# Kernel optimization log

Measured on AMD Instinct MI355X. Metric: run time of the kernel, lower is better.

## Reference

```python
import math
import jax, jax.numpy as jnp
import numpy as np

NUM_HEADS = 16
QUERY_SIZE = 1024
SEQ = 2048
HEAD = QUERY_SIZE // NUM_HEADS  # qk_size = vo_size = 64


def setup_inputs() -> dict:
    key = jax.random.key(0)
    ks = jax.random.split(key, 8)
    s = 0.02
    query = jax.random.normal(ks[0], (SEQ, QUERY_SIZE), jnp.float32)
    key_ = jax.random.normal(ks[1], (SEQ, QUERY_SIZE), jnp.float32)
    value = jax.random.normal(ks[2], (SEQ, QUERY_SIZE), jnp.float32)
    # causal mask (mask='causal' with state=None -> offset 0)
    mask = jnp.tril(jnp.ones((SEQ, SEQ), dtype=bool))
    Wq = jax.random.normal(ks[3], (QUERY_SIZE, QUERY_SIZE), jnp.float32) * s
    Wk = jax.random.normal(ks[4], (QUERY_SIZE, QUERY_SIZE), jnp.float32) * s
    Wv = jax.random.normal(ks[5], (QUERY_SIZE, QUERY_SIZE), jnp.float32) * s
    Wo = jax.random.normal(ks[6], (QUERY_SIZE, QUERY_SIZE), jnp.float32) * s
    return {"query": query, "key_": key_, "value": value, "mask": mask,
            "Wq": Wq, "Wk": Wk, "Wv": Wv, "Wo": Wo}


def reference(query, key_, value, mask, Wq, Wk, Wv, Wo):
    H, D = NUMS = NUM_HEADS, HEAD
    S = query.shape[0]
    inv_sqrt_d = 1.0 / math.sqrt(D)
    # per-token linear projections, split into heads: [S, H, D]
    q = (query @ Wq.T).reshape(S, H, D)
    k = (key_ @ Wk.T).reshape(S, H, D)
    v = (value @ Wv.T).reshape(S, H, D)
    # NOTE: original divides BOTH q and k by sqrt(d) (effective 1/d scaling)
    q = q * inv_sqrt_d
    k = k * inv_sqrt_d
    # logits per head: [H, S, S]
    logits = jnp.einsum('shd,Shd->hsS', q, k)
    logits = jnp.where(mask[None, :, :], logits, jnp.finfo(logits.dtype).min)
    # per-head GLOBAL max subtraction, softmax in fp32, cast back (faithful)
    m = jnp.max(logits, axis=(1, 2), keepdims=True)
    weights = jax.nn.softmax((logits - m).astype(jnp.float32), axis=-1).astype(query.dtype)
    attn = jnp.einsum('hsS,ShD->shD', weights, v).reshape(S, H * D)
    return attn @ Wo.T
```

## Files before the change

### kernel.cpp

```cpp
#include <hip/hip_runtime.h>
#include <hip/hip_bf16.h>

typedef __bf16 bf16_t;
typedef __bf16 bf16x8 __attribute__((ext_vector_type(8)));
typedef float f32x4 __attribute__((ext_vector_type(4)));

#define MFMA(A, B, C) __builtin_amdgcn_mfma_f32_16x16x32_bf16(A, B, C, 0, 0, 0)

#define GLL16(g, l) __builtin_amdgcn_global_load_lds(                      \
    (const __attribute__((address_space(1))) void*)(g),                    \
    (__attribute__((address_space(3))) void*)(l), 16, 0, 0)

__global__ __launch_bounds__(256) void cvt_all(
    const float* __restrict__ q, const float* __restrict__ k, const float* __restrict__ v,
    const float* __restrict__ wq, const float* __restrict__ wk,
    const float* __restrict__ wv, const float* __restrict__ wo,
    bf16_t* __restrict__ xq, bf16_t* __restrict__ xk, bf16_t* __restrict__ xv,
    bf16_t* __restrict__ ywq, bf16_t* __restrict__ ywk,
    bf16_t* __restrict__ ywv, bf16_t* __restrict__ ywo)
{
  const long gid = (long)blockIdx.x * 256 + threadIdx.x;
  const float* s; bf16_t* d; long off; float sc = 1.0f;
  if (gid < 262144)       { s = q;  d = xq;  off = gid; }
  else if (gid < 524288)  { s = k;  d = xk;  off = gid - 262144; }
  else if (gid < 786432)  { s = v;  d = xv;  off = gid - 524288; }
  else if (gid < 917504)  { s = wq; d = ywq; off = gid - 786432;  sc = 0.125f; }
  else if (gid < 1048576) { s = wk; d = ywk; off = gid - 917504;  sc = 0.125f * 1.44269504f; }
  else if (gid < 1179648) { s = wv; d = ywv; off = gid - 1048576; }
  else                    { s = wo; d = ywo; off = gid - 1179648; }
  const float* p = s + off * 8;
  float4 a = *(const float4*)p, b = *(const float4*)(p + 4);
  bf16x8 o;
  o[0] = (bf16_t)(a.x * sc); o[1] = (bf16_t)(a.y * sc);
  o[2] = (bf16_t)(a.z * sc); o[3] = (bf16_t)(a.w * sc);
  o[4] = (bf16_t)(b.x * sc); o[5] = (bf16_t)(b.y * sc);
  o[6] = (bf16_t)(b.z * sc); o[7] = (bf16_t)(b.w * sc);
  *(bf16x8*)(d + off * 8) = o;
}

__device__ __forceinline__ void gemm_core(const bf16_t* __restrict__ A,
                                          const bf16_t* __restrict__ W,
                                          int bm, int bn,
                                          bf16_t (&As)[2][128 * 64],
                                          bf16_t (&Bs)[2][64 * 64],
                                          f32x4 (&acc)[4][2])
{
  const int tid = threadIdx.x, lane = tid & 63, wave = tid >> 6;
  const int l15 = lane & 15, l4 = lane >> 4, l7 = l15 & 7;
  const int wm = (wave >> 1) * 64, wn = (wave & 1) * 32;

  auto stage = [&](int buf, int k0) {
#pragma unroll
    for (int i = 0; i < 4; ++i) {
      const int id = i * 256 + tid, row = id >> 3, cph = id & 7;
      GLL16(A + (size_t)(bm + row) * 1024 + k0 + 8 * (cph ^ (row & 7)),
            &As[buf][(i * 256 + wave * 64) * 8]);
    }
#pragma unroll
    for (int i = 0; i < 2; ++i) {
      const int id = i * 256 + tid, row = id >> 3, cph = id & 7;
      GLL16(W + (size_t)(bn + row) * 1024 + k0 + 8 * (cph ^ (row & 7)),
            &Bs[buf][(i * 256 + wave * 64) * 8]);
    }
  };

  stage(0, 0);
#pragma unroll
  for (int s = 0; s < 16; ++s) {
    if (s + 1 < 16) stage((s + 1) & 1, (s + 1) * 64);
    __syncthreads();
    const bf16_t* as = As[s & 1];
    const bf16_t* bs = Bs[s & 1];
#pragma unroll
    for (int ks = 0; ks < 2; ++ks) {
      bf16x8 af[4], bfr[2];
#pragma unroll
      for (int i = 0; i < 4; ++i)
        af[i] = *(const bf16x8*)(&as[(wm + i * 16 + l15) * 64 + 8 * ((ks * 4 + l4) ^ l7)]);
#pragma unroll
      for (int j = 0; j < 2; ++j)
        bfr[j] = *(const bf16x8*)(&bs[(wn + j * 16 + l15) * 64 + 8 * ((ks * 4 + l4) ^ l7)]);
#pragma unroll
      for (int i = 0; i < 4; ++i)
#pragma unroll
        for (int j = 0; j < 2; ++j)
          acc[i][j] = MFMA(af[i], bfr[j], acc[i][j]);
    }
    __syncthreads();
  }
}

__global__ __launch_bounds__(256) void gemm_qkv(
    const bf16_t* __restrict__ xq, const bf16_t* __restrict__ xk, const bf16_t* __restrict__ xv,
    const bf16_t* __restrict__ ywq, const bf16_t* __restrict__ ywk, const bf16_t* __restrict__ ywv,
    bf16_t* __restrict__ qo, bf16_t* __restrict__ ko, bf16_t* __restrict__ vt)
{
  __shared__ __align__(16) bf16_t As[2][128 * 64];
  __shared__ __align__(16) bf16_t Bs[2][64 * 64];
  const int z = blockIdx.z;
  const bf16_t* A = z == 0 ? xq : z == 1 ? xk : xv;
  const bf16_t* W = z == 0 ? ywq : z == 1 ? ywk : ywv;
  const int bm = blockIdx.x * 128, bn = blockIdx.y * 64;
  f32x4 acc[4][2] = {};
  gemm_core(A, W, bm, bn, As, Bs, acc);
  const int tid = threadIdx.x, lane = tid & 63, wave = tid >> 6;
  const int l15 = lane & 15, l4 = lane >> 4;
  const int wm = (wave >> 1) * 64, wn = (wave & 1) * 32;
  if (z < 2) {
    bf16_t* C = z == 0 ? qo : ko;
#pragma unroll
    for (int i = 0; i < 4; ++i)
#pragma unroll
      for (int j = 0; j < 2; ++j)
#pragma unroll
        for (int r = 0; r < 4; ++r)
          C[(size_t)(bm + wm + i * 16 + 4 * l4 + r) * 1024 + bn + wn + j * 16 + l15] =
              (bf16_t)acc[i][j][r];
  } else {
#pragma unroll
    for (int i = 0; i < 4; ++i)
#pragma unroll
      for (int j = 0; j < 2; ++j)
#pragma unroll
        for (int r = 0; r < 4; ++r)
          vt[(size_t)(bn + wn + j * 16 + l15) * 2048 + bm + wm + i * 16 + 4 * l4 + r] =
              (bf16_t)acc[i][j][r];
  }
}

__global__ __launch_bounds__(256) void gemm_out(
    const bf16_t* __restrict__ ctx, const bf16_t* __restrict__ ywo, float* __restrict__ out)
{
  __shared__ __align__(16) bf16_t As[2][128 * 64];
  __shared__ __align__(16) bf16_t Bs[2][64 * 64];
  const int bm = blockIdx.x * 128, bn = blockIdx.y * 64;
  f32x4 acc[4][2] = {};
  gemm_core(ctx, ywo, bm, bn, As, Bs, acc);
  const int tid = threadIdx.x, lane = tid & 63, wave = tid >> 6;
  const int l15 = lane & 15, l4 = lane >> 4;
  const int wm = (wave >> 1) * 64, wn = (wave & 1) * 32;
#pragma unroll
  for (int i = 0; i < 4; ++i)
#pragma unroll
    for (int j = 0; j < 2; ++j)
#pragma unroll
      for (int r = 0; r < 4; ++r)
        out[(size_t)(bm + wm + i * 16 + 4 * l4 + r) * 1024 + bn + wn + j * 16 + l15] =
            acc[i][j][r];
}

__global__ __launch_bounds__(512) void attn512v2(
    const bf16_t* __restrict__ Qb, const bf16_t* __restrict__ Kb,
    const bf16_t* __restrict__ Vt, bf16_t* __restrict__ Ctx)
{
  __shared__ __align__(16) char pool[16384 + 16384 + 10240 + 256];
  bf16_t* KsP = (bf16_t*)pool;
  bf16_t* VsP = (bf16_t*)(pool + 16384);
  bf16_t* PsP = (bf16_t*)(pool + 32768);
  float*  Osc = (float*)pool;
  float*  Dsc = (float*)(pool + 43008);

  const int bid = blockIdx.x;
  const int qt = 31 - (bid >> 4);
  const int h = bid & 15;
  const int hoff = h * 64;
  const int tid = threadIdx.x, lane = tid & 63, wave = tid >> 6;
  const int qg = wave & 3, kh = wave >> 2;
  const int l15 = lane & 15, l4 = lane >> 4, l7 = l15 & 7;

  const int qb = qt * 64;
  const int nch = qt + 1;
  const int qmin = qb + 16 * qg;

  bf16x8 qf[2];
#pragma unroll
  for (int kc = 0; kc < 2; ++kc)
    qf[kc] = *(const bf16x8*)(Qb + (size_t)(qb + 16 * qg + l15) * 1024 + hoff + 32 * kc + 8 * l4);

  f32x4 oacc[4] = {};
  float den[4] = {0.f, 0.f, 0.f, 0.f};

  bf16x8 rk, rv;
  auto issue = [&](int c) {
    const int t0 = c * 64;
    const int kr = tid >> 3, kc = tid & 7;
    rk = *(const bf16x8*)(Kb + (size_t)(t0 + kr) * 1024 + hoff + 8 * kc);
    rv = *(const bf16x8*)(Vt + (size_t)(hoff + kr) * 2048 + t0 + 8 * kc);
  };
  auto commit = [&](int buf) {
    const int kr = tid >> 3, kc = tid & 7;
    *(bf16x8*)(&KsP[buf * 4096 + kr * 64 + 8 * (kc ^ (kr & 7))]) = rk;
    *(bf16x8*)(&VsP[buf * 4096 + kr * 64 + 8 * (kc ^ (kr & 7))]) = rv;
  };

  bf16_t* Pw = &PsP[wave * 640];
  auto PROC = [&](int cur, int c, auto masked) {
    const int tb = c * 64 + kh * 32;
    if (tb > qmin + 15) return;
    const bf16_t* Ksb = KsP + cur * 4096;
    const bf16_t* Vsb = VsP + cur * 4096;
    f32x4 sv[2] = {};
#pragma unroll
    for (int tf = 0; tf < 2; ++tf) {
      const int krow = 32 * kh + 16 * tf + l15;
      bf16x8 kf0 = *(const bf16x8*)(&Ksb[krow * 64 + 8 * (l4 ^ l7)]);
      bf16x8 kf1 = *(const bf16x8*)(&Ksb[krow * 64 + 8 * ((4 + l4) ^ l7)]);
      sv[tf] = MFMA(qf[0], kf0, sv[tf]);
      sv[tf] = MFMA(qf[1], kf1, sv[tf]);
    }
#pragma unroll
    for (int tf = 0; tf < 2; ++tf) {
      const int t = tb + 16 * tf + l15;
#pragma unroll
      for (int r = 0; r < 4; ++r) {
        float p = __builtin_amdgcn_exp2f(sv[tf][r]);
        if constexpr (decltype(masked)::value) {
          const int qq = qb + 16 * qg + 4 * l4 + r;
          p = (t <= qq) ? p : 0.0f;
        }
        den[r] += p;
        Pw[(4 * l4 + r) * 40 + 16 * tf + l15] = (bf16_t)p;
      }
    }
    asm volatile("s_waitcnt lgkmcnt(0)" ::: "memory");
    bf16x8 pa = *(const bf16x8*)(&Pw[l15 * 40 + 8 * l4]);
#pragma unroll
    for (int df = 0; df < 4; ++df) {
      const int vrow = 16 * df + l15;
      bf16x8 vf = *(const bf16x8*)(&Vsb[vrow * 64 + 8 * ((4 * kh + l4) ^ l7)]);
      oacc[df] = MFMA(pa, vf, oacc[df]);
    }
  };

  issue(0);
  commit(0);
  int cur = 0;
  for (int c = 0; c < nch; ++c) {
    const bool pre = (c + 1 < nch);
    if (pre) issue(c + 1);
    __syncthreads();
    const int tb = c * 64 + kh * 32;
    if (tb + 31 <= qmin)
      PROC(cur, c, std::integral_constant<bool, false>{});
    else
      PROC(cur, c, std::integral_constant<bool, true>{});
    if (pre) commit(cur ^ 1);
    cur ^= 1;
  }

#pragma unroll
  for (int r = 0; r < 4; ++r)
#pragma unroll
    for (int m = 1; m < 16; m <<= 1)
      den[r] += __shfl_xor(den[r], m, 64);

  __syncthreads();
  if (kh == 1) {
    const int rl = qg * 16 + 4 * l4;
#pragma unroll
    for (int r = 0; r < 4; ++r) {
#pragma unroll
      for (int df = 0; df < 4; ++df)
        Osc[(rl + r) * 66 + 16 * df + l15] = oacc[df][r];
      if (l15 == 0) Dsc[rl + r] = den[r];
    }
  }
  __syncthreads();
  if (kh == 0) {
#pragma unroll
    for (int r = 0; r < 4; ++r) {
      const int row = qg * 16 + 4 * l4 + r;
      const float inv = 1.0f / (den[r] + Dsc[row]);
#pragma unroll
      for (int df = 0; df < 4; ++df) {
        const int col = 16 * df + l15;
        const float s = oacc[df][r] + Osc[row * 66 + col];
        Ctx[(size_t)(qb + row) * 1024 + hoff + col] = (bf16_t)(s * inv);
      }
    }
  }
}

extern "C" void kernel_launch(void* const* d_in, const int* in_sizes, int n_in,
                              void* d_out, int out_size, void* d_ws, size_t ws_size,
                              hipStream_t stream)
{
  const float* query = (const float*)d_in[0];
  const float* key_  = (const float*)d_in[1];
  const float* value = (const float*)d_in[2];
  const float* Wq = (const float*)d_in[4];
  const float* Wk = (const float*)d_in[5];
  const float* Wv = (const float*)d_in[6];
  const float* Wo = (const float*)d_in[7];
  float* out = (float*)d_out;

  const size_t SE = (size_t)2048 * 1024, EE = (size_t)1024 * 1024;
  bf16_t* xq  = (bf16_t*)d_ws;
  bf16_t* xk  = xq + SE;
  bf16_t* xv  = xk + SE;
  bf16_t* wq  = xv + SE;
  bf16_t* wk  = wq + EE;
  bf16_t* wv  = wk + EE;
  bf16_t* wo  = wv + EE;
  bf16_t* qo  = wo + EE;
  bf16_t* ko  = qo + SE;
  bf16_t* vt  = ko + SE;
  bf16_t* ctx = vt + SE;

  cvt_all<<<5120, 256, 0, stream>>>(query, key_, value, Wq, Wk, Wv, Wo,
                                    xq, xk, xv, wq, wk, wv, wo);
  gemm_qkv<<<dim3(16, 16, 3), 256, 0, stream>>>(xq, xk, xv, wq, wk, wv, qo, ko, vt);
  attn512v2<<<512, 512, 0, stream>>>(qo, ko, vt, ctx);
  gemm_out<<<dim3(16, 16), 256, 0, stream>>>(ctx, wo, out);
}
```

Before: 75.58 us.

## Rewrite attention as register-resident 32x32 MFMA kernel with split-K waves

Replaces the LDS-staged attention kernel with one where each wave loads K and V fragments straight from global memory into registers, double-buffered. It uses 32x32x16 MFMAs and moves the P tile between lane halves with shuffles instead of through LDS. Query tiles shrink to 32 rows, giving 1024 blocks of 4 waves, and each wave takes every fourth key chunk; partial outputs and denominators are reduced through shared memory at the end. This removes per-chunk __syncthreads and LDS traffic, at the cost of redundant global/L2 loads across waves and more registers.

```diff
diff --git a/kernel.cpp b/kernel.cpp
--- a/kernel.cpp
+++ b/kernel.cpp
@@ -4,12 +4,25 @@
 typedef __bf16 bf16_t;
 typedef __bf16 bf16x8 __attribute__((ext_vector_type(8)));
 typedef float f32x4 __attribute__((ext_vector_type(4)));
+typedef float f32x16 __attribute__((ext_vector_type(16)));
 
 #define MFMA(A, B, C) __builtin_amdgcn_mfma_f32_16x16x32_bf16(A, B, C, 0, 0, 0)
+#define MFMA32(A, B, C) __builtin_amdgcn_mfma_f32_32x32x16_bf16(A, B, C, 0, 0, 0)
 
 #define GLL16(g, l) __builtin_amdgcn_global_load_lds(                      \
     (const __attribute__((address_space(1))) void*)(g),                    \
     (__attribute__((address_space(3))) void*)(l), 16, 0, 0)
+
+static __device__ __forceinline__ bf16x8 frag4(unsigned a, unsigned b, unsigned c, unsigned d) {
+  union { unsigned u[4]; bf16x8 v; } x;
+  x.u[0] = a; x.u[1] = b; x.u[2] = c; x.u[3] = d;
+  return x.v;
+}
+static __device__ __forceinline__ unsigned pack2b(bf16_t lo, bf16_t hi) {
+  union { bf16_t b[2]; unsigned u; } x;
+  x.b[0] = lo; x.b[1] = hi;
+  return x.u;
+}
 
 __global__ __launch_bounds__(256) void cvt_all(
     const float* __restrict__ q, const float* __restrict__ k, const float* __restrict__ v,
@@ -149,134 +162,119 @@
             acc[i][j][r];
 }
 
-__global__ __launch_bounds__(512) void attn512v2(
+__global__ __launch_bounds__(256) void attn_reg(
     const bf16_t* __restrict__ Qb, const bf16_t* __restrict__ Kb,
     const bf16_t* __restrict__ Vt, bf16_t* __restrict__ Ctx)
 {
-  __shared__ __align__(16) char pool[16384 + 16384 + 10240 + 256];
-  bf16_t* KsP = (bf16_t*)pool;
-  bf16_t* VsP = (bf16_t*)(pool + 16384);
-  bf16_t* PsP = (bf16_t*)(pool + 32768);
-  float*  Osc = (float*)pool;
-  float*  Dsc = (float*)(pool + 43008);
+  __shared__ float Osc[3][32 * 64];
+  __shared__ float Dsc[4][32];
 
   const int bid = blockIdx.x;
-  const int qt = 31 - (bid >> 4);
+  const int u = 63 - (bid >> 4);
   const int h = bid & 15;
   const int hoff = h * 64;
-  const int tid = threadIdx.x, lane = tid & 63, wave = tid >> 6;
-  const int qg = wave & 3, kh = wave >> 2;
-  const int l15 = lane & 15, l4 = lane >> 4, l7 = l15 & 7;
-
-  const int qb = qt * 64;
-  const int nch = qt + 1;
-  const int qmin = qb + 16 * qg;
-
-  bf16x8 qf[2];
-#pragma unroll
-  for (int kc = 0; kc < 2; ++kc)
-    qf[kc] = *(const bf16x8*)(Qb + (size_t)(qb + 16 * qg + l15) * 1024 + hoff + 32 * kc + 8 * l4);
-
-  f32x4 oacc[4] = {};
-  float den[4] = {0.f, 0.f, 0.f, 0.f};
-
-  bf16x8 rk, rv;
-  auto issue = [&](int c) {
-    const int t0 = c * 64;
-    const int kr = tid >> 3, kc = tid & 7;
-    rk = *(const bf16x8*)(Kb + (size_t)(t0 + kr) * 1024 + hoff + 8 * kc);
-    rv = *(const bf16x8*)(Vt + (size_t)(hoff + kr) * 2048 + t0 + 8 * kc);
+  const int lane = threadIdx.x & 63, tph = threadIdx.x >> 6;
+  const int l31 = lane & 31, hi = lane >> 5;
+
+  const int qb = u * 32;
+  const int q_lane = qb + l31;
+  const int nch = u + 1;
+  const bf16_t* Kh = Kb + hoff;
+  const bf16_t* Vh = Vt + (size_t)hoff * 2048;
+
+  bf16x8 qf[4];
+#pragma unroll
+  for (int st = 0; st < 4; ++st)
+    qf[st] = *(const bf16x8*)(Qb + (size_t)(qb + l31) * 1024 + hoff + 16 * st + 8 * hi);
+
+  f32x16 o0 = {}, o1 = {};
+  float den = 0.f;
+
+  bf16x8 kfA[4], vfA[4], kfB[4], vfB[4];
+  auto LOAD = [&](bf16x8 (&kf)[4], bf16x8 (&vf)[4], int c) {
+    const int t0 = c * 32;
+#pragma unroll
+    for (int st = 0; st < 4; ++st)
+      kf[st] = *(const bf16x8*)(Kh + (size_t)(t0 + l31) * 1024 + 16 * st + 8 * hi);
+#pragma unroll
+    for (int db = 0; db < 2; ++db)
+#pragma unroll
+      for (int kh = 0; kh < 2; ++kh)
+        vf[db * 2 + kh] = *(const bf16x8*)(Vh + (size_t)(32 * db + l31) * 2048 + t0 + 16 * kh + 8 * hi);
   };
-  auto commit = [&](int buf) {
-    const int kr = tid >> 3, kc = tid & 7;
-    *(bf16x8*)(&KsP[buf * 4096 + kr * 64 + 8 * (kc ^ (kr & 7))]) = rk;
-    *(bf16x8*)(&VsP[buf * 4096 + kr * 64 + 8 * (kc ^ (kr & 7))]) = rv;
+
+  auto PROC = [&](const bf16x8 (&kf)[4], const bf16x8 (&vf)[4], int c) {
+    const int t0 = c * 32;
+    f32x16 sv = {};
+#pragma unroll
+    for (int st = 0; st < 4; ++st)
+      sv = MFMA32(kf[st], qf[st], sv);
+    const bool diag = (c + 1 == nch);
+    bf16_t pb[16];
+#pragma unroll
+    for (int reg = 0; reg < 16; ++reg) {
+      const int t = t0 + (reg & 3) + 8 * (reg >> 2) + 4 * hi;
+      float e = __builtin_amdgcn_exp2f(sv[reg]);
+      if (diag && t > q_lane) e = 0.f;
+      const bf16_t b = (bf16_t)e;
+      pb[reg] = b;
+      den += (float)b;
+    }
+    unsigned pk[8];
+#pragma unroll
+    for (int i = 0; i < 8; ++i) pk[i] = pack2b(pb[2 * i], pb[2 * i + 1]);
+    const unsigned r0a = __shfl_xor((int)(hi ? pk[0] : pk[2]), 32, 64);
+    const unsigned r0b = __shfl_xor((int)(hi ? pk[1] : pk[3]), 32, 64);
+    const unsigned r1a = __shfl_xor((int)(hi ? pk[4] : pk[6]), 32, 64);
+    const unsigned r1b = __shfl_xor((int)(hi ? pk[5] : pk[7]), 32, 64);
+    const bf16x8 pf0 = hi ? frag4(r0a, r0b, pk[2], pk[3]) : frag4(pk[0], pk[1], r0a, r0b);
+    const bf16x8 pf1 = hi ? frag4(r1a, r1b, pk[6], pk[7]) : frag4(pk[4], pk[5], r1a, r1b);
+    o0 = MFMA32(pf0, vf[0], o0);
+    o0 = MFMA32(pf1, vf[1], o0);
+    o1 = MFMA32(pf0, vf[2], o1);
+    o1 = MFMA32(pf1, vf[3], o1);
   };
 
-  bf16_t* Pw = &PsP[wave * 640];
-  auto PROC = [&](int cur, int c, auto masked) {
-    const int tb = c * 64 + kh * 32;
-    if (tb > qmin + 15) return;
-    const bf16_t* Ksb = KsP + cur * 4096;
-    const bf16_t* Vsb = VsP + cur * 4096;
-    f32x4 sv[2] = {};
-#pragma unroll
-    for (int tf = 0; tf < 2; ++tf) {
-      const int krow = 32 * kh + 16 * tf + l15;
-      bf16x8 kf0 = *(const bf16x8*)(&Ksb[krow * 64 + 8 * (l4 ^ l7)]);
-      bf16x8 kf1 = *(const bf16x8*)(&Ksb[krow * 64 + 8 * ((4 + l4) ^ l7)]);
-      sv[tf] = MFMA(qf[0], kf0, sv[tf]);
-      sv[tf] = MFMA(qf[1], kf1, sv[tf]);
-    }
-#pragma unroll
-    for (int tf = 0; tf < 2; ++tf) {
-      const int t = tb + 16 * tf + l15;
-#pragma unroll
-      for (int r = 0; r < 4; ++r) {
-        float p = __builtin_amdgcn_exp2f(sv[tf][r]);
-        if constexpr (decltype(masked)::value) {
-          const int qq = qb + 16 * qg + 4 * l4 + r;
-          p = (t <= qq) ? p : 0.0f;
-        }
-        den[r] += p;
-        Pw[(4 * l4 + r) * 40 + 16 * tf + l15] = (bf16_t)p;
-      }
-    }
+  int c = tph;
+  if (c < nch) {
+    LOAD(kfA, vfA, c);
+    while (true) {
+      if (c + 4 < nch) LOAD(kfB, vfB, c + 4);
+      PROC(kfA, vfA, c);
+      c += 4;
+      if (c >= nch) break;
+      if (c + 4 < nch) LOAD(kfA, vfA, c + 4);
+      PROC(kfB, vfB, c);
+      c += 4;
+      if (c >= nch) break;
+    }
+  }
+
+  den += __shfl_xor(den, 32, 64);
+
+  if (hi == 0) Dsc[tph][l31] = den;
+  if (tph > 0) {
+#pragma unroll
+    for (int reg = 0; reg < 16; ++reg) {
+      const int qr = (reg & 3) + 8 * (reg >> 2) + 4 * hi;
+      Osc[tph - 1][qr * 64 + l31] = o0[reg];
+      Osc[tph - 1][qr * 64 + 32 + l31] = o1[reg];
+    }
+  }
+  __syncthreads();
+  if (tph == 0) {
+    const float dtot = Dsc[0][l31] + Dsc[1][l31] + Dsc[2][l31] + Dsc[3][l31];
+    if (hi == 0) Dsc[0][l31] = dtot;
     asm volatile("s_waitcnt lgkmcnt(0)" ::: "memory");
-    bf16x8 pa = *(const bf16x8*)(&Pw[l15 * 40 + 8 * l4]);
-#pragma unroll
-    for (int df = 0; df < 4; ++df) {
-      const int vrow = 16 * df + l15;
-      bf16x8 vf = *(const bf16x8*)(&Vsb[vrow * 64 + 8 * ((4 * kh + l4) ^ l7)]);
-      oacc[df] = MFMA(pa, vf, oacc[df]);
-    }
-  };
-
-  issue(0);
-  commit(0);
-  int cur = 0;
-  for (int c = 0; c < nch; ++c) {
-    const bool pre = (c + 1 < nch);
-    if (pre) issue(c + 1);
-    __syncthreads();
-    const int tb = c * 64 + kh * 32;
-    if (tb + 31 <= qmin)
-      PROC(cur, c, std::integral_constant<bool, false>{});
-    else
-      PROC(cur, c, std::integral_constant<bool, true>{});
-    if (pre) commit(cur ^ 1);
-    cur ^= 1;
-  }
-
-#pragma unroll
-  for (int r = 0; r < 4; ++r)
-#pragma unroll
-    for (int m = 1; m < 16; m <<= 1)
-      den[r] += __shfl_xor(den[r], m, 64);
-
-  __syncthreads();
-  if (kh == 1) {
-    const int rl = qg * 16 + 4 * l4;
-#pragma unroll
-    for (int r = 0; r < 4; ++r) {
-#pragma unroll
-      for (int df = 0; df < 4; ++df)
-        Osc[(rl + r) * 66 + 16 * df + l15] = oacc[df][r];
-      if (l15 == 0) Dsc[rl + r] = den[r];
-    }
-  }
-  __syncthreads();
-  if (kh == 0) {
-#pragma unroll
-    for (int r = 0; r < 4; ++r) {
-      const int row = qg * 16 + 4 * l4 + r;
-      const float inv = 1.0f / (den[r] + Dsc[row]);
-#pragma unroll
-      for (int df = 0; df < 4; ++df) {
-        const int col = 16 * df + l15;
-        const float s = oacc[df][r] + Osc[row * 66 + col];
-        Ctx[(size_t)(qb + row) * 1024 + hoff + col] = (bf16_t)(s * inv);
-      }
+    __builtin_amdgcn_sched_barrier(0);
+#pragma unroll
+    for (int reg = 0; reg < 16; ++reg) {
+      const int qr = (reg & 3) + 8 * (reg >> 2) + 4 * hi;
+      const float s0 = o0[reg] + Osc[0][qr * 64 + l31] + Osc[1][qr * 64 + l31] + Osc[2][qr * 64 + l31];
+      const float s1 = o1[reg] + Osc[0][qr * 64 + 32 + l31] + Osc[1][qr * 64 + 32 + l31] + Osc[2][qr * 64 + 32 + l31];
+      const float inv = 1.0f / Dsc[0][qr];
+      Ctx[(size_t)(qb + qr) * 1024 + hoff + l31] = (bf16_t)(s0 * inv);
+      Ctx[(size_t)(qb + qr) * 1024 + hoff + 32 + l31] = (bf16_t)(s1 * inv);
     }
   }
 }
@@ -310,6 +308,6 @@
   cvt_all<<<5120, 256, 0, stream>>>(query, key_, value, Wq, Wk, Wv, Wo,
                                     xq, xk, xv, wq, wk, wv, wo);
   gemm_qkv<<<dim3(16, 16, 3), 256, 0, stream>>>(xq, xk, xv, wq, wk, wv, qo, ko, vt);
-  attn512v2<<<512, 512, 0, stream>>>(qo, ko, vt, ctx);
+  attn_reg<<<1024, 256, 0, stream>>>(qo, ko, vt, ctx);
   gemm_out<<<dim3(16, 16), 256, 0, stream>>>(ctx, wo, out);
 }
```

Measured after the change: 85.89 us. 13.6% more time.
